# Optimization experiments

Measured on AMD Instinct MI355X. Metric: run time of the kernel, lower is better.

The kernel has to match this reference:

```python
import jax, jax.numpy as jnp
import numpy as np

LEAKY_ALPHA = 0.2  # LeakyReLU negative slope from init arg `alpha`


def setup_inputs() -> dict:
    key = jax.random.key(0)
    k1, k2, k3, k4 = jax.random.split(key, 4)
    B, N, Fin, Fout = 8, 2048, 256, 256
    h = jax.random.normal(k1, (B, N, Fin), dtype=jnp.float32)
    adj = jax.random.randint(k2, (N, N), 0, 2, dtype=jnp.int32)
    W = jax.random.normal(k3, (Fin, Fout), dtype=jnp.float32) * (1.414 * (6.0 / (Fin + Fout)) ** 0.5)
    a = jax.random.normal(k4, (2 * Fout, 1), dtype=jnp.float32) * (1.414 * (6.0 / (2 * Fout + 1)) ** 0.5)
    return {"h": h, "adj": adj, "W": W, "a": a}


def reference(h, adj, W, a):
    # h: (B, N, Fin), adj: (N, N) int {0,1}, W: (Fin, Fout), a: (2*Fout, 1)
    Fout = W.shape[1]
    Wh = jnp.einsum('bnf,fo->bno', h, W)            # (B, N, Fout)
    a1 = a[:Fout, 0]                                  # attends to target node i
    a2 = a[Fout:, 0]                                  # attends to source node j
    # a^T [Wh_i || Wh_j] == (Wh_i . a1) + (Wh_j . a2); LeakyReLU applied after, as in original
    s_i = Wh @ a1                                     # (B, N)
    s_j = Wh @ a2                                     # (B, N)
    e = jax.nn.leaky_relu(s_i[:, :, None] + s_j[:, None, :], negative_slope=LEAKY_ALPHA)  # (B, N, N)
    N = Wh.shape[1]
    mask = (adj > 0) | jnp.eye(N, dtype=bool)         # adjacency + self-loops
    e = jnp.where(mask[None, :, :], e, -jnp.inf)
    attention = jax.nn.softmax(e, axis=-1)            # dropout is identity in eval
    attention = jnp.nan_to_num(attention, nan=0.0)
    h_prime = jnp.einsum('bij,bjo->bio', attention, Wh)  # (B, N, Fout)
    return jax.nn.elu(h_prime)                        # concat=True -> ELU
```

## Files before the change

### kernel.cpp

```cpp
#include <hip/hip_runtime.h>

typedef unsigned short u16;
typedef unsigned int   u32;
typedef unsigned long long u64;

typedef __bf16 bf16x8 __attribute__((ext_vector_type(8)));
typedef float  f32x4  __attribute__((ext_vector_type(4)));

#define MFMA_BF16(a,b,c) __builtin_amdgcn_mfma_f32_16x16x32_bf16((a),(b),(c),0,0,0)

#define GLOAD_LDS16(g, l) __builtin_amdgcn_global_load_lds( \
    (const __attribute__((address_space(1))) void*)(g), \
    (__attribute__((address_space(3))) void*)(l), 16, 0, 0)

__device__ __forceinline__ float bf2f(u16 u) {
    return __uint_as_float(((u32)u) << 16);
}
__device__ __forceinline__ u16 f2bf(float x) {
    u32 u = __float_as_uint(x);
    u += 0x7fffu + ((u >> 16) & 1u);
    return (u16)(u >> 16);
}
__device__ __forceinline__ float ldany(const void* p, size_t i, int f32) {
    return f32 ? ((const float*)p)[i] : bf2f(((const u16*)p)[i]);
}
__device__ __forceinline__ int detect_f32(const u32* hw) {
    u32 w = hw[threadIdx.x & 63];
    int e = (w >> 23) & 0xFF;
    u64 m = __ballot(e >= 64 && e <= 190);
    return __popcll(m) >= 32 ? 1 : 0;
}

__global__ __launch_bounds__(256) void k0(const void* __restrict__ w, const void* __restrict__ a,
                                          u16* __restrict__ wt, float* __restrict__ wa1,
                                          float* __restrict__ wa2, const u32* __restrict__ hw) {
    int f32 = detect_f32(hw);
    int k = blockIdx.x, o = threadIdx.x;
    float wv = ldany(w, (size_t)k * 256 + o, f32);
    wt[o * 256 + k] = f2bf(wv);
    float p1 = wv * ldany(a, o, f32);
    float p2 = wv * ldany(a, 256 + o, f32);
    for (int d = 32; d; d >>= 1) { p1 += __shfl_down(p1, d); p2 += __shfl_down(p2, d); }
    __shared__ float s1[4], s2[4];
    int wid = o >> 6, lane = o & 63;
    if (lane == 0) { s1[wid] = p1; s2[wid] = p2; }
    __syncthreads();
    if (o == 0) { wa1[k] = s1[0] + s1[1] + s1[2] + s1[3]; wa2[k] = s2[0] + s2[1] + s2[2] + s2[3]; }
}

__global__ __launch_bounds__(256) void k1(const void* __restrict__ h,
                                          const float* __restrict__ wa1, const float* __restrict__ wa2,
                                          const int* __restrict__ adj,
                                          float* __restrict__ si, float* __restrict__ sj,
                                          u64* __restrict__ mb64) {
    int f32 = detect_f32((const u32*)h);
    int t = threadIdx.x;
    int wv = t >> 6, lane = t & 63;
    int row = blockIdx.x * 4 + wv;
    size_t base = (size_t)row * 256;
    float a1 = 0.f, a2 = 0.f;
    for (int p = 0; p < 4; p++) {
        int f = lane + p * 64;
        float hv = ldany(h, base + f, f32);
        a1 += hv * wa1[f];
        a2 += hv * wa2[f];
    }
    for (int d = 32; d; d >>= 1) { a1 += __shfl_down(a1, d); a2 += __shfl_down(a2, d); }
    if (lane == 0) { si[row] = a1; sj[row] = a2; }
    #pragma unroll
    for (int q = 0; q < 4; q++) {
        int idx = blockIdx.x * 16 + wv * 4 + q;
        int mrow = idx >> 5, c = idx & 31;
        int j = c * 64 + lane;
        bool bit = (adj[(size_t)mrow * 2048 + j] > 0) || (j == mrow);
        u64 m = __ballot(bit);
        if (lane == 0) mb64[(size_t)mrow * 32 + c] = m;
    }
}

struct __align__(16) K2LDS {
    u16 At[64 * 68];
    union { u16 Bt[256 * 68]; u16 Ct[256 * 68]; };
};
__global__ __launch_bounds__(256) void k2(const void* __restrict__ h, const u16* __restrict__ wt,
                                          u16* __restrict__ whbt) {
    __shared__ K2LDS L;
    int f32 = detect_f32((const u32*)h);
    int m0 = blockIdx.x * 64;
    int b  = m0 >> 11;
    int n0 = m0 & 2047;
    int t = threadIdx.x;
    int wid = t >> 6, lane = t & 63, ln = lane & 15, qd = lane >> 4;

    f32x4 acc[4][4];
    for (int mi = 0; mi < 4; mi++)
        for (int ni = 0; ni < 4; ni++)
            acc[mi][ni] = (f32x4){0.f, 0.f, 0.f, 0.f};

    for (int c = 0; c < 4; c++) {
        int k0c = c * 64;
        for (int p = 0; p < 2; p++) {
            int r = (t >> 3) + p * 32, s = t & 7;
            if (f32) {
                const float* src = (const float*)h + (size_t)(m0 + r) * 256 + k0c + s * 8;
                f32x4 x0 = *(const f32x4*)src;
                f32x4 x1 = *(const f32x4*)(src + 4);
                u16 v[8];
                for (int q = 0; q < 4; q++) { v[q] = f2bf(x0[q]); v[4 + q] = f2bf(x1[q]); }
                *(uint4*)&L.At[r * 68 + s * 8] = *(uint4*)v;
            } else {
                *(uint4*)&L.At[r * 68 + s * 8] =
                    *(const uint4*)((const u16*)h + (size_t)(m0 + r) * 256 + k0c + s * 8);
            }
        }
        for (int p = 0; p < 8; p++) {
            int f = (t >> 3) + p * 32, s = t & 7;
            *(uint4*)&L.Bt[f * 68 + s * 8] =
                *(const uint4*)(wt + (size_t)f * 256 + k0c + s * 8);
        }
        __syncthreads();
        for (int ks = 0; ks < 2; ks++) {
            bf16x8 af[4], bfr[4];
            for (int mi = 0; mi < 4; mi++)
                af[mi] = *(const bf16x8*)&L.At[(mi * 16 + ln) * 68 + ks * 32 + qd * 8];
            for (int ni = 0; ni < 4; ni++)
                bfr[ni] = *(const bf16x8*)&L.Bt[(wid * 64 + ni * 16 + ln) * 68 + ks * 32 + qd * 8];
            for (int mi = 0; mi < 4; mi++)
                for (int ni = 0; ni < 4; ni++)
                    acc[mi][ni] = MFMA_BF16(af[mi], bfr[ni], acc[mi][ni]);
        }
        __syncthreads();
    }
    for (int mi = 0; mi < 4; mi++) {
        for (int ni = 0; ni < 4; ni++) {
            int f = wid * 64 + ni * 16 + ln;
            int n = mi * 16 + qd * 4;
            u16 v[4];
            for (int r = 0; r < 4; r++) v[r] = f2bf(acc[mi][ni][r]);
            *(uint2*)&L.Ct[f * 68 + n] = *(uint2*)v;
        }
    }
    __syncthreads();
    {
        int fr = t;
        size_t base = (size_t)b * 524288 + (size_t)fr * 2048 + n0;
        #pragma unroll
        for (int s = 0; s < 8; s++) {
            int qsrc = s ^ (fr & 7);
            uint4 v = *(uint4*)&L.Ct[fr * 68 + qsrc * 8];
            *(uint4*)(whbt + base + s * 8) = v;
        }
    }
}

__global__ __launch_bounds__(512) void k3n(const float* __restrict__ sig, const float* __restrict__ sjg,
                                           float* __restrict__ u1g, float* __restrict__ u2g,
                                           u32* __restrict__ vpackg, u16* __restrict__ sjbfg) {
    int b = blockIdx.x;
    int t = threadIdx.x;
    const float* sjb = sjg + (size_t)b * 2048;
    float mx = -3.4e38f;
    #pragma unroll
    for (int p = 0; p < 4; p++) mx = fmaxf(mx, sjb[t + p * 512]);
    for (int d = 32; d; d >>= 1) mx = fmaxf(mx, __shfl_xor(mx, d));
    __shared__ float wmax[8];
    int wid = t >> 6, lane = t & 63;
    if (lane == 0) wmax[wid] = mx;
    __syncthreads();
    float Mb = fmaxf(fmaxf(fmaxf(wmax[0], wmax[1]), fmaxf(wmax[2], wmax[3])),
                     fmaxf(fmaxf(wmax[4], wmax[5]), fmaxf(wmax[6], wmax[7])));
    #pragma unroll
    for (int p = 0; p < 4; p++) {
        int j = t + p * 512;
        float sjv = sjb[j];
        float vj  = __expf(sjv - Mb);
        float v2j = __expf(0.2f * (sjv - Mb));
        vpackg[b * 2048 + j] = (u32)f2bf(vj) | ((u32)f2bf(v2j) << 16);
        sjbfg[b * 2048 + j]  = f2bf(sjv);
        float siv = sig[b * 2048 + j];
        float x = siv + Mb;
        float K = fmaxf(x, 0.2f * x);
        u1g[b * 2048 + j] = __expf(x - K);
        u2g[b * 2048 + j] = __expf(0.2f * x - K);
    }
}

struct __align__(16) K4LDS {
    u32   vpack[2048];
    u16   sjb[2048];
    u64   mw[64 * 33];
    float u1[64], u2[64], inv[64], nsi[64];
    float lred[512];
    u16   Pt[2][4096];
    u16   Wt[2][16384];
};
__global__ __launch_bounds__(512, 2) void k4(const float* __restrict__ sig,
                                             const float* __restrict__ u1g, const float* __restrict__ u2g,
                                             const u32* __restrict__ vpackg, const u16* __restrict__ sjbfg,
                                             const u64* __restrict__ mb64, const u16* __restrict__ whbt,
                                             void* __restrict__ out, const void* __restrict__ hdet) {
    __shared__ K4LDS L;
    int f32 = detect_f32((const u32*)hdet);
    int b  = blockIdx.x & 7;
    int i0 = (blockIdx.x >> 3) * 64;
    int t = threadIdx.x;
    int wid = t >> 6, lane = t & 63, ln = lane & 15, qd = lane >> 4;
    int wm = wid & 1, wn = wid >> 1;
    const u16* wb = whbt + (size_t)b * 524288;
    float lacc = 0.f;

    #define ISSUE_DMA(cc, bb) do {                                          \
        int j0_ = (cc) * 64;                                                \
        _Pragma("unroll")                                                   \
        for (int q = 0; q < 4; q++) {                                       \
            int k_ = wid * 4 + q;                                           \
            int fl_ = k_ * 8 + (lane >> 3);                                 \
            const u16* g_ = wb + (size_t)fl_ * 2048 + j0_ + (lane & 7) * 8; \
            GLOAD_LDS16(g_, &L.Wt[bb][k_ * 512]);                           \
        }                                                                   \
    } while (0)

    #define PGEN(cc, bb) do {                                               \
        int r_ = t & 63, o_ = t >> 6;                                       \
        int jb_ = (cc) * 64 + o_ * 8;                                       \
        uint4 pkA_ = *(const uint4*)&L.vpack[jb_];                          \
        uint4 pkB_ = *(const uint4*)&L.vpack[jb_ + 4];                      \
        uint4 sj4_ = *(const uint4*)&L.sjb[jb_];                            \
        u32 mb_ = (u32)(L.mw[r_ * 33 + (cc)] >> (o_ * 8)) & 0xffu;          \
        float u1_ = L.u1[r_], u2_ = L.u2[r_], nsi_ = L.nsi[r_];             \
        u32 pr_[4];                                                         \
        _Pragma("unroll")                                                   \
        for (int pk = 0; pk < 4; pk++) {                                    \
            u32 vw0_ = (pk == 0) ? pkA_.x : (pk == 1) ? pkA_.z              \
                     : (pk == 2) ? pkB_.x : pkB_.z;                         \
            u32 vw1_ = (pk == 0) ? pkA_.y : (pk == 1) ? pkA_.w              \
                     : (pk == 2) ? pkB_.y : pkB_.w;                         \
            u32 sw_ = (pk == 0) ? sj4_.x : (pk == 1) ? sj4_.y               \
                     : (pk == 2) ? sj4_.z : sj4_.w;                         \
            float sj0_ = __uint_as_float(sw_ << 16);                        \
            float sj1_ = __uint_as_float(sw_ & 0xffff0000u);                \
            float p0_, p1_;                                                 \
            {                                                               \
                bool pos = sj0_ > nsi_;                                     \
                float vv = __uint_as_float(pos ? (vw0_ << 16)               \
                                               : ((vw0_ >> 16) << 16));     \
                p0_ = (pos ? u1_ : u2_) * vv;                               \
                p0_ = ((mb_ >> (2 * pk)) & 1u) ? p0_ : 0.f;                 \
            }                                                               \
            {                                                               \
                bool pos = sj1_ > nsi_;                                     \
                float vv = __uint_as_float(pos ? (vw1_ << 16)               \
                                               : ((vw1_ >> 16) << 16));     \
                p1_ = (pos ? u1_ : u2_) * vv;                               \
                p1_ = ((mb_ >> (2 * pk + 1)) & 1u) ? p1_ : 0.f;             \
            }                                                               \
            lacc += p0_ + p1_;                                              \
            pr_[pk] = __builtin_amdgcn_perm(__float_as_uint(p1_),           \
                                            __float_as_uint(p0_),           \
                                            0x07060302u);                   \
        }                                                                   \
        *(uint4*)&L.Pt[bb][(o_ * 64 + r_) * 8] = *(uint4*)pr_;              \
    } while (0)

    ISSUE_DMA(0, 0);
    for (int p = 0; p < 4; p++) { int idx = t + p * 512; L.vpack[idx] = vpackg[b * 2048 + idx]; }
    for (int p = 0; p < 2; p++) { int idx = t + p * 512;
        ((u32*)L.sjb)[idx] = ((const u32*)(sjbfg + (size_t)b * 2048))[idx]; }
    for (int p = 0; p < 4; p++) {
        int idx = t + p * 512;
        int r = idx >> 5, c = idx & 31;
        L.mw[r * 33 + c] = mb64[(size_t)(i0 + r) * 32 + c];
    }
    if (t < 64) {
        int row = b * 2048 + i0 + t;
        L.u1[t] = u1g[row]; L.u2[t] = u2g[row]; L.nsi[t] = -sig[row];
    }
    __syncthreads();
    PGEN(0, 0);

    f32x4 acc[2][4];
    for (int mi = 0; mi < 2; mi++)
        for (int ni = 0; ni < 4; ni++)
            acc[mi][ni] = (f32x4){0.f, 0.f, 0.f, 0.f};

    for (int c = 0; c < 32; c++) {
        int cur = c & 1, nxt = cur ^ 1;
        __syncthreads();
        if (c < 31) { ISSUE_DMA(c + 1, nxt); PGEN(c + 1, nxt); }
        #pragma unroll
        for (int ks = 0; ks < 2; ks++) {
            bf16x8 af[2], bfr[4];
            #pragma unroll
            for (int mi = 0; mi < 2; mi++)
                af[mi] = *(const bf16x8*)&L.Pt[cur][((ks * 4 + qd) * 64 + wm * 32 + mi * 16 + ln) * 8];
            #pragma unroll
            for (int ni = 0; ni < 4; ni++) {
                int fl = wn * 64 + ni * 16 + ln;
                int swc = (ks * 4 + qd) ^ (fl & 7);
                bfr[ni] = *(const bf16x8*)&L.Wt[cur][fl * 64 + swc * 8];
            }
            #pragma unroll
            for (int mi = 0; mi < 2; mi++)
                #pragma unroll
                for (int ni = 0; ni < 4; ni++)
                    acc[mi][ni] = MFMA_BF16(af[mi], bfr[ni], acc[mi][ni]);
        }
    }

    __syncthreads();
    L.lred[t] = lacc;
    __syncthreads();
    if (t < 64) {
        float s = 0.f;
        #pragma unroll
        for (int q = 0; q < 8; q++) s += L.lred[q * 64 + t];
        L.inv[t] = 1.0f / s;
    }
    __syncthreads();

    for (int mi = 0; mi < 2; mi++) {
        int rl0 = wm * 32 + mi * 16 + qd * 4;
        for (int ni = 0; ni < 4; ni++) {
            int fg = wn * 64 + ni * 16 + ln;
            for (int reg = 0; reg < 4; reg++) {
                int rl = rl0 + reg;
                float hp = acc[mi][ni][reg] * L.inv[rl];
                float y = hp > 0.f ? hp : (__expf(hp) - 1.f);
                size_t idx = (size_t)(b * 2048 + i0 + rl) * 256 + fg;
                if (f32) ((float*)out)[idx] = y;
                else     ((u16*)out)[idx]   = f2bf(y);
            }
        }
    }
    #undef ISSUE_DMA
    #undef PGEN
}

extern "C" void kernel_launch(void* const* d_in, const int* in_sizes, int n_in,
                              void* d_out, int out_size, void* d_ws, size_t ws_size,
                              hipStream_t stream) {
    const void* h   = d_in[0];
    const int*  adj = (const int*)d_in[1];
    const void* W   = d_in[2];
    const void* a   = d_in[3];

    char* ws = (char*)d_ws;
    u16*   WT    = (u16*)  (ws + 0);
    float* si    = (float*)(ws + 131072);
    float* sj    = (float*)(ws + 196608);
    float* u1    = (float*)(ws + 262144);
    float* u2    = (float*)(ws + 327680);
    u32*   vpack = (u32*)  (ws + 458752);
    u16*   sjbf  = (u16*)  (ws + 524288);
    u64*   mb64  = (u64*)  (ws + 557056);
    u16*   whbt  = (u16*)  (ws + 1081344);
    float* Wa1   = (float*)(ws + 9469952);
    float* Wa2   = (float*)(ws + 9470976);

    k0 <<<dim3(256),  dim3(256), 0, stream>>>(W, a, WT, Wa1, Wa2, (const u32*)h);
    k1 <<<dim3(4096), dim3(256), 0, stream>>>(h, Wa1, Wa2, adj, si, sj, mb64);
    k2 <<<dim3(256),  dim3(256), 0, stream>>>(h, WT, whbt);
    k3n<<<dim3(8),    dim3(512), 0, stream>>>(si, sj, u1, u2, vpack, sjbf);
    k4 <<<dim3(256),  dim3(512), 0, stream>>>(si, u1, u2, vpack, sjbf, mb64, whbt, d_out, h);
}
```

Baseline: 143.2 us.

## Load attention B operand directly to registers with smaller row tiles in k4

k4 now uses 32-row tiles and 256-thread blocks (512 blocks instead of 256). Each wave owns 64 output features and reads its Wh^T fragments straight from global memory into a double-buffered register array, replacing the LDS staging via global_load_lds. The k2 transpose output no longer uses the XOR swizzle because the LDS layout that needed it is gone. This removes LDS traffic and the B-tile staging, and adds blocks to the grid for parallelism. In exchange, each block reuses the B tile across fewer rows (32 instead of 64), which doubles global reads of Wh, and the register-held fragments raise register pressure.

Measured after the change: 164.6 us. 1.15x slower.

```diff
diff --git a/kernel.cpp b/kernel.cpp
--- a/kernel.cpp
+++ b/kernel.cpp
@@ -8,10 +8,6 @@
 typedef float  f32x4  __attribute__((ext_vector_type(4)));
 
 #define MFMA_BF16(a,b,c) __builtin_amdgcn_mfma_f32_16x16x32_bf16((a),(b),(c),0,0,0)
-
-#define GLOAD_LDS16(g, l) __builtin_amdgcn_global_load_lds( \
-    (const __attribute__((address_space(1))) void*)(g), \
-    (__attribute__((address_space(3))) void*)(l), 16, 0, 0)
 
 __device__ __forceinline__ float bf2f(u16 u) {
     return __uint_as_float(((u32)u) << 16);
@@ -146,8 +142,7 @@
         size_t base = (size_t)b * 524288 + (size_t)fr * 2048 + n0;
         #pragma unroll
         for (int s = 0; s < 8; s++) {
-            int qsrc = s ^ (fr & 7);
-            uint4 v = *(uint4*)&L.Ct[fr * 68 + qsrc * 8];
+            uint4 v = *(uint4*)&L.Ct[fr * 68 + s * 8];
             *(uint4*)(whbt + base + s * 8) = v;
         }
     }
@@ -188,13 +183,12 @@
 struct __align__(16) K4LDS {
     u32   vpack[2048];
     u16   sjb[2048];
-    u64   mw[64 * 33];
-    float u1[64], u2[64], inv[64], nsi[64];
-    float lred[512];
-    u16   Pt[2][4096];
-    u16   Wt[2][16384];
+    u64   mw[32 * 33];
+    float u1[32], u2[32], nsi[32], inv[32];
+    float lred[256];
+    u16   Pt[2][2048];
 };
-__global__ __launch_bounds__(512, 2) void k4(const float* __restrict__ sig,
+__global__ __launch_bounds__(256, 2) void k4(const float* __restrict__ sig,
                                              const float* __restrict__ u1g, const float* __restrict__ u2g,
                                              const u32* __restrict__ vpackg, const u16* __restrict__ sjbfg,
                                              const u64* __restrict__ mb64, const u16* __restrict__ whbt,
@@ -202,26 +196,25 @@
     __shared__ K4LDS L;
     int f32 = detect_f32((const u32*)hdet);
     int b  = blockIdx.x & 7;
-    int i0 = (blockIdx.x >> 3) * 64;
+    int i0 = (blockIdx.x >> 3) * 32;
     int t = threadIdx.x;
     int wid = t >> 6, lane = t & 63, ln = lane & 15, qd = lane >> 4;
-    int wm = wid & 1, wn = wid >> 1;
-    const u16* wb = whbt + (size_t)b * 524288;
+    const u16* wb = whbt + (size_t)b * 524288 + (size_t)wid * 64 * 2048;
     float lacc = 0.f;
 
-    #define ISSUE_DMA(cc, bb) do {                                          \
+    bf16x8 br[2][8];
+    #define LOAD_B(cc, bb) do {                                             \
         int j0_ = (cc) * 64;                                                \
         _Pragma("unroll")                                                   \
-        for (int q = 0; q < 4; q++) {                                       \
-            int k_ = wid * 4 + q;                                           \
-            int fl_ = k_ * 8 + (lane >> 3);                                 \
-            const u16* g_ = wb + (size_t)fl_ * 2048 + j0_ + (lane & 7) * 8; \
-            GLOAD_LDS16(g_, &L.Wt[bb][k_ * 512]);                           \
-        }                                                                   \
+        for (int ni = 0; ni < 4; ni++)                                      \
+            _Pragma("unroll")                                               \
+            for (int ks = 0; ks < 2; ks++)                                  \
+                br[bb][ni * 2 + ks] = *(const bf16x8*)(wb +                 \
+                    (size_t)(ni * 16 + ln) * 2048 + j0_ + ks * 32 + qd * 8);\
     } while (0)
 
     #define PGEN(cc, bb) do {                                               \
-        int r_ = t & 63, o_ = t >> 6;                                       \
+        int r_ = t & 31, o_ = t >> 5;                                       \
         int jb_ = (cc) * 64 + o_ * 8;                                       \
         uint4 pkA_ = *(const uint4*)&L.vpack[jb_];                          \
         uint4 pkB_ = *(const uint4*)&L.vpack[jb_ + 4];                      \
@@ -259,19 +252,19 @@
                                             __float_as_uint(p0_),           \
                                             0x07060302u);                   \
         }                                                                   \
-        *(uint4*)&L.Pt[bb][(o_ * 64 + r_) * 8] = *(uint4*)pr_;              \
+        *(uint4*)&L.Pt[bb][t * 8] = *(uint4*)pr_;                           \
     } while (0)
 
-    ISSUE_DMA(0, 0);
-    for (int p = 0; p < 4; p++) { int idx = t + p * 512; L.vpack[idx] = vpackg[b * 2048 + idx]; }
-    for (int p = 0; p < 2; p++) { int idx = t + p * 512;
+    LOAD_B(0, 0);
+    for (int p = 0; p < 8; p++) { int idx = t + p * 256; L.vpack[idx] = vpackg[b * 2048 + idx]; }
+    for (int p = 0; p < 4; p++) { int idx = t + p * 256;
         ((u32*)L.sjb)[idx] = ((const u32*)(sjbfg + (size_t)b * 2048))[idx]; }
     for (int p = 0; p < 4; p++) {
-        int idx = t + p * 512;
+        int idx = t + p * 256;
         int r = idx >> 5, c = idx & 31;
         L.mw[r * 33 + c] = mb64[(size_t)(i0 + r) * 32 + c];
     }
-    if (t < 64) {
+    if (t < 32) {
         int row = b * 2048 + i0 + t;
         L.u1[t] = u1g[row]; L.u2[t] = u2g[row]; L.nsi[t] = -sig[row];
     }
@@ -283,47 +276,46 @@
         for (int ni = 0; ni < 4; ni++)
             acc[mi][ni] = (f32x4){0.f, 0.f, 0.f, 0.f};
 
-    for (int c = 0; c < 32; c++) {
-        int cur = c & 1, nxt = cur ^ 1;
-        __syncthreads();
-        if (c < 31) { ISSUE_DMA(c + 1, nxt); PGEN(c + 1, nxt); }
-        #pragma unroll
-        for (int ks = 0; ks < 2; ks++) {
-            bf16x8 af[2], bfr[4];
-            #pragma unroll
-            for (int mi = 0; mi < 2; mi++)
-                af[mi] = *(const bf16x8*)&L.Pt[cur][((ks * 4 + qd) * 64 + wm * 32 + mi * 16 + ln) * 8];
-            #pragma unroll
-            for (int ni = 0; ni < 4; ni++) {
-                int fl = wn * 64 + ni * 16 + ln;
-                int swc = (ks * 4 + qd) ^ (fl & 7);
-                bfr[ni] = *(const bf16x8*)&L.Wt[cur][fl * 64 + swc * 8];
-            }
-            #pragma unroll
-            for (int mi = 0; mi < 2; mi++)
-                #pragma unroll
-                for (int ni = 0; ni < 4; ni++)
-                    acc[mi][ni] = MFMA_BF16(af[mi], bfr[ni], acc[mi][ni]);
-        }
+    #define STEP(c, cur, nxt) do {                                          \
+        __syncthreads();                                                    \
+        if ((c) < 31) { LOAD_B((c) + 1, nxt); PGEN((c) + 1, nxt); }         \
+        _Pragma("unroll")                                                   \
+        for (int ks = 0; ks < 2; ks++) {                                    \
+            bf16x8 af[2];                                                   \
+            _Pragma("unroll")                                               \
+            for (int mi = 0; mi < 2; mi++)                                  \
+                af[mi] = *(const bf16x8*)&L.Pt[cur][((ks * 4 + qd) * 32 +   \
+                                                     mi * 16 + ln) * 8];    \
+            _Pragma("unroll")                                               \
+            for (int mi = 0; mi < 2; mi++)                                  \
+                _Pragma("unroll")                                           \
+                for (int ni = 0; ni < 4; ni++)                              \
+                    acc[mi][ni] = MFMA_BF16(af[mi], br[cur][ni * 2 + ks],   \
+                                            acc[mi][ni]);                   \
+        }                                                                   \
+    } while (0)
+
+    for (int cc = 0; cc < 16; cc++) {
+        STEP(2 * cc,     0, 1);
+        STEP(2 * cc + 1, 1, 0);
     }
 
     __syncthreads();
     L.lred[t] = lacc;
     __syncthreads();
-    if (t < 64) {
+    if (t < 32) {
         float s = 0.f;
         #pragma unroll
-        for (int q = 0; q < 8; q++) s += L.lred[q * 64 + t];
+        for (int q = 0; q < 8; q++) s += L.lred[q * 32 + t];
         L.inv[t] = 1.0f / s;
     }
     __syncthreads();
 
     for (int mi = 0; mi < 2; mi++) {
-        int rl0 = wm * 32 + mi * 16 + qd * 4;
         for (int ni = 0; ni < 4; ni++) {
-            int fg = wn * 64 + ni * 16 + ln;
+            int fg = wid * 64 + ni * 16 + ln;
             for (int reg = 0; reg < 4; reg++) {
-                int rl = rl0 + reg;
+                int rl = mi * 16 + qd * 4 + reg;
                 float hp = acc[mi][ni][reg] * L.inv[rl];
                 float y = hp > 0.f ? hp : (__expf(hp) - 1.f);
                 size_t idx = (size_t)(b * 2048 + i0 + rl) * 256 + fg;
@@ -332,8 +324,9 @@
             }
         }
     }
-    #undef ISSUE_DMA
+    #undef LOAD_B
     #undef PGEN
+    #undef STEP
 }
 
 extern "C" void kernel_launch(void* const* d_in, const int* in_sizes, int n_in,
@@ -361,5 +354,5 @@
     k1 <<<dim3(4096), dim3(256), 0, stream>>>(h, Wa1, Wa2, adj, si, sj, mb64);
     k2 <<<dim3(256),  dim3(256), 0, stream>>>(h, WT, whbt);
     k3n<<<dim3(8),    dim3(512), 0, stream>>>(si, sj, u1, u2, vpack, sjbf);
-    k4 <<<dim3(256),  dim3(512), 0, stream>>>(si, u1, u2, vpack, sjbf, mb64, whbt, d_out, h);
-}
+    k4 <<<dim3(512),  dim3(256), 0, stream>>>(si, u1, u2, vpack, sjbf, mb64, whbt, d_out, h);
+}
```
